# Optimization experiments

Hardware: AMD Instinct MI355X
Metric: run time of the kernel (lower is better)

The kernel has to match this reference:

```python
import jax, jax.numpy as jnp
import numpy as np

B, S, D, H = 4, 4096, 1024, 16
DH = D // H  # 64
EPS = 1e-6


def setup_inputs() -> dict:
    key = jax.random.key(0)
    ks = jax.random.split(key, 6)
    scale = 1.0 / np.sqrt(D).astype(np.float32)
    x = jax.random.normal(ks[0], (B, S, D), jnp.float32)
    # packed cache: rows 0..DH-1 = KV state S0, row DH = normalizer z0 (kept positive)
    state_cache = jax.random.uniform(ks[1], (B, H, DH + 1, DH), jnp.float32)
    Wq = jax.random.normal(ks[2], (D, D), jnp.float32) * scale
    Wk = jax.random.normal(ks[3], (D, D), jnp.float32) * scale
    Wv = jax.random.normal(ks[4], (D, D), jnp.float32) * scale
    Wo = jax.random.normal(ks[5], (D, D), jnp.float32) * scale
    return {"x": x, "state_cache": state_cache, "Wq": Wq, "Wk": Wk, "Wv": Wv, "Wo": Wo}


def reference(x, state_cache, Wq, Wk, Wv, Wo):
    b, s, d = x.shape
    h, dh = H, d // H

    def heads(t):  # [b,s,d] -> [s,b,h,dh] (seq-major for scan)
        return t.reshape(b, s, h, dh).transpose(1, 0, 2, 3)

    phi = lambda t: jax.nn.elu(t) + 1.0  # positive feature map
    q = phi(heads(x @ Wq))
    k = phi(heads(x @ Wk))
    v = heads(x @ Wv)

    S0 = state_cache[:, :, :dh, :]   # [b,h,dh,dh]
    z0 = state_cache[:, :, dh, :]    # [b,h,dh]

    def step(carry, inp):
        Sst, z = carry
        qt, kt, vt = inp  # each [b,h,dh]
        Sst = Sst + jnp.einsum('bhd,bhe->bhde', kt, vt)
        z = z + kt
        num = jnp.einsum('bhd,bhde->bhe', qt, Sst)            # [b,h,dh]
        den = jnp.einsum('bhd,bhd->bh', qt, z)[..., None]     # [b,h,1]
        return (Sst, z), num / (den + EPS)

    _, outs = jax.lax.scan(step, (S0, z0), (q, k, v))  # outs: [s,b,h,dh]
    out = outs.transpose(1, 0, 2, 3).reshape(b, s, d)
    return out @ Wo
```

## Files before the change

kernel.cpp:

```cpp
#include <hip/hip_runtime.h>

#define B_ 4
#define S_ 4096
#define D_ 1024
#define H_ 16
#define DH 64
#define CHUNK 64
#define NC (S_ / CHUNK)
#define BH (B_ * H_)
#define STATE_N 4160
#define EPS 1e-6f

typedef __bf16 bf16;
typedef __bf16 bf16x8 __attribute__((ext_vector_type(8)));
typedef __bf16 bf16x4 __attribute__((ext_vector_type(4)));
typedef float v4f __attribute__((ext_vector_type(4)));

#define MFMA16(a, b, c) __builtin_amdgcn_mfma_f32_16x16x32_bf16(a, b, c, 0, 0, 0)

__device__ __forceinline__ void load_lds16(const bf16* g, bf16* l) {
  __builtin_amdgcn_global_load_lds(
      (const __attribute__((address_space(1))) unsigned int*)g,
      (__attribute__((address_space(3))) unsigned int*)l, 16, 0, 0);
}

__global__ __launch_bounds__(256) void cvt_f32_bf16(const float* __restrict__ in,
                                                    bf16* __restrict__ out) {
  const size_t i = ((size_t)blockIdx.x * 256 + threadIdx.x) * 8;
  float4 a = *(const float4*)(in + i);
  float4 b = *(const float4*)(in + i + 4);
  bf16x8 o;
  o[0] = (bf16)a.x; o[1] = (bf16)a.y; o[2] = (bf16)a.z; o[3] = (bf16)a.w;
  o[4] = (bf16)b.x; o[5] = (bf16)b.y; o[6] = (bf16)b.z; o[7] = (bf16)b.w;
  *(bf16x8*)(out + i) = o;
}

__global__ __launch_bounds__(256) void transpose_w4(
    const float* __restrict__ w0, const float* __restrict__ w1,
    const float* __restrict__ w2, const float* __restrict__ w3,
    bf16* __restrict__ out) {
  __shared__ float tile[32][33];
  const int z = blockIdx.z;
  const float* in = (z == 0) ? w0 : (z == 1) ? w1 : (z == 2) ? w2 : w3;
  bf16* o = out + (size_t)z * D_ * D_;
  const int bx = blockIdx.x * 32, by = blockIdx.y * 32;
  const int tx = threadIdx.x & 31, ty = threadIdx.x >> 5;
#pragma unroll
  for (int i = 0; i < 32; i += 8)
    tile[ty + i][tx] = in[(size_t)(by + ty + i) * D_ + bx + tx];
  __syncthreads();
#pragma unroll
  for (int i = 0; i < 32; i += 8)
    o[(size_t)(bx + ty + i) * D_ + by + tx] = (bf16)tile[tx][ty + i];
}

__global__ __launch_bounds__(256) void gemm_nt(const bf16* __restrict__ A,
                                               const bf16* __restrict__ BT,
                                               bf16* __restrict__ o0,
                                               bf16* __restrict__ o1,
                                               bf16* __restrict__ o2,
                                               float* __restrict__ of) {
  constexpr int TM = 128, BK = 32;
  constexpr int CLD = 132;
  __shared__ __align__(16) char smem[32768];
  float* Cl = (float*)smem;

  const int tid = threadIdx.x;
  const int wave = tid >> 6, lane = tid & 63;
  const int quad = lane >> 4, l16 = lane & 15;
  const int bm = blockIdx.x * TM;
  const int zz = blockIdx.y >> 3;
  const int colg = (blockIdx.y & 7) * 128;
  const int wm = (wave & 1) * 64, wn = (wave >> 1) * 64;
  const int act = (of == nullptr) && (zz < 2);
  bf16* ob = (zz == 0) ? o0 : (zz == 1) ? o1 : o2;

  const int srow = wave * 16 + (lane >> 2);
  const int sgrp = ((lane & 3) - ((lane >> 2) >> 1)) & 3;
  const bf16* gA0 = A + (size_t)(bm + srow) * D_ + sgrp * 8;
  const bf16* gA1 = gA0 + (size_t)64 * D_;
  const bf16* gB0 = BT + ((size_t)blockIdx.y * 128 + srow) * D_ + sgrp * 8;
  const bf16* gB1 = gB0 + (size_t)64 * D_;

  int offA[4], offB[4];
#pragma unroll
  for (int i = 0; i < 4; i++) {
    const int pg = (quad + (l16 >> 1)) & 3;
    offA[i] = (wm + i * 16 + l16) * BK + pg * 8;
    offB[i] = (wn + i * 16 + l16) * BK + pg * 8;
  }

  v4f zero = {0.f, 0.f, 0.f, 0.f};
  v4f acc[4][4];
#pragma unroll
  for (int i = 0; i < 4; i++)
#pragma unroll
    for (int j = 0; j < 4; j++) acc[i][j] = zero;

  auto stage = [&](int ks, int s) {
    bf16* As = (bf16*)(smem + s * 16384);
    bf16* Bs = As + 4096;
    const int ko = ks * BK;
    load_lds16(gA0 + ko, As + wave * 16 * BK);
    load_lds16(gA1 + ko, As + (64 + wave * 16) * BK);
    load_lds16(gB0 + ko, Bs + wave * 16 * BK);
    load_lds16(gB1 + ko, Bs + (64 + wave * 16) * BK);
  };
  auto compute = [&](int s) {
    const bf16* As = (const bf16*)(smem + s * 16384);
    const bf16* Bs = As + 4096;
    bf16x8 af[4], bfr[4];
#pragma unroll
    for (int i = 0; i < 4; i++) af[i] = *(const bf16x8*)&As[offA[i]];
#pragma unroll
    for (int j = 0; j < 4; j++) bfr[j] = *(const bf16x8*)&Bs[offB[j]];
#pragma unroll
    for (int i = 0; i < 4; i++)
#pragma unroll
      for (int j = 0; j < 4; j++) acc[i][j] = MFMA16(af[i], bfr[j], acc[i][j]);
  };

  constexpr int NK = D_ / BK;
  stage(0, 0);
  __syncthreads();
  for (int k = 0; k < NK; k += 2) {
    if (k + 1 < NK) stage(k + 1, 1);
    compute(0);
    __syncthreads();
    if (k + 2 < NK) stage(k + 2, 0);
    compute(1);
    __syncthreads();
  }

  const int lr = (wave & 1) * 16 + quad * 4;
  const int rrow = tid >> 3;
  const int rseg = (tid & 7) * 16;
  const int grow = bm + (rrow >> 4) * 64 + (rrow & 15);
#pragma unroll
  for (int i = 0; i < 4; i++) {
    __syncthreads();
#pragma unroll
    for (int j = 0; j < 4; j++) {
      const int col = wn + j * 16 + l16;
#pragma unroll
      for (int r = 0; r < 4; r++) {
        float x = acc[i][j][r];
        if (act) x = x > 0.f ? x + 1.f : __expf(x);
        Cl[(lr + r) * CLD + col] = x;
      }
    }
    __syncthreads();
    const float* src = &Cl[rrow * CLD + rseg];
    if (of) {
      float* dst = of + (size_t)(grow + i * 16) * D_ + colg + rseg;
#pragma unroll
      for (int u = 0; u < 4; u++)
        *(float4*)(dst + u * 4) = *(const float4*)(src + u * 4);
    } else {
      bf16x8 q0, q1;
#pragma unroll
      for (int u = 0; u < 8; u++) { q0[u] = (bf16)src[u]; q1[u] = (bf16)src[8 + u]; }
      bf16* dst = ob + (size_t)(grow + i * 16) * D_ + colg + rseg;
      *(bf16x8*)dst = q0;
      *(bf16x8*)(dst + 8) = q1;
    }
  }
}

__global__ __launch_bounds__(256) void chunk_kv(const bf16* __restrict__ kb,
                                                const bf16* __restrict__ vb,
                                                float* __restrict__ states) {
  constexpr int LD = 88;
  __shared__ bf16 Kl[CHUNK * LD];
  __shared__ bf16 Vl[CHUNK * LD];
  const int tid = threadIdx.x;
  const int c = blockIdx.x, bh = blockIdx.y;
  const int b = bh >> 4, h = bh & 15;
  const size_t gbase = ((size_t)(b * S_ + c * CHUNK)) * D_ + h * DH;
#pragma unroll
  for (int rep = 0; rep < 2; rep++) {
    int flat = tid + rep * 256;
    int r = flat >> 3, sg = (flat & 7) * 8;
    *(bf16x8*)&Kl[r * LD + sg] = *(const bf16x8*)(kb + gbase + (size_t)r * D_ + sg);
    *(bf16x8*)&Vl[r * LD + sg] = *(const bf16x8*)(vb + gbase + (size_t)r * D_ + sg);
  }
  __syncthreads();
  const int d0 = (tid >> 4) * 4, e0 = (tid & 15) * 4;
  float acc[4][4] = {};
  for (int t = 0; t < CHUNK; t++) {
    bf16x4 k4 = *(const bf16x4*)&Kl[t * LD + d0];
    bf16x4 v4 = *(const bf16x4*)&Vl[t * LD + e0];
    float kf[4], vf[4];
#pragma unroll
    for (int i = 0; i < 4; i++) { kf[i] = (float)k4[i]; vf[i] = (float)v4[i]; }
#pragma unroll
    for (int i = 0; i < 4; i++)
#pragma unroll
      for (int j = 0; j < 4; j++) acc[i][j] += kf[i] * vf[j];
  }
  float* out = states + ((size_t)bh * NC + c) * STATE_N;
#pragma unroll
  for (int i = 0; i < 4; i++)
#pragma unroll
    for (int j = 0; j < 4; j++) out[(d0 + i) * 64 + (e0 + j)] = acc[i][j];
  if (tid < 64) {
    float zs = 0.f;
    for (int t = 0; t < CHUNK; t++) zs += (float)Kl[t * LD + tid];
    out[4096 + tid] = zs;
  }
}

__global__ __launch_bounds__(256) void state_prefix(const float* __restrict__ sc,
                                                    float* __restrict__ states) {
  const int bh = blockIdx.x;
  const int e = blockIdx.y * 256 + threadIdx.x;
  if (e >= STATE_N) return;
  const float* scb = sc + (size_t)bh * (DH + 1) * DH;
  float run = scb[e];
  float* p = states + (size_t)bh * NC * STATE_N + e;
  for (int c = 0; c < NC; c++) {
    float tmp = p[(size_t)c * STATE_N];
    p[(size_t)c * STATE_N] = run;
    run += tmp;
  }
}

__global__ __launch_bounds__(256) void attn_pass2(
    const bf16* __restrict__ qb, const bf16* __restrict__ kb,
    const bf16* __restrict__ vb, const float* __restrict__ states,
    bf16* __restrict__ ao) {
  constexpr int LD = 88;
  __shared__ bf16 Ql[CHUNK * LD];
  __shared__ bf16 Kl[CHUNK * LD];
  __shared__ bf16 VT[DH * LD];
  __shared__ bf16 S0T[DH * LD];
  __shared__ bf16 Pl[CHUNK * LD];
  __shared__ float denl[CHUNK];
  __shared__ float z0l[DH];
  const int tid = threadIdx.x;
  const int wave = tid >> 6, lane = tid & 63;
  const int quad = lane >> 4, l16 = lane & 15;
  const int c = blockIdx.x, bh = blockIdx.y;
  const int b = bh >> 4, h = bh & 15;
  const size_t gbase = ((size_t)(b * S_ + c * CHUNK)) * D_ + h * DH;

#pragma unroll
  for (int rep = 0; rep < 2; rep++) {
    int flat = tid + rep * 256;
    int r = flat >> 3, sg = (flat & 7) * 8;
    *(bf16x8*)&Ql[r * LD + sg] = *(const bf16x8*)(qb + gbase + (size_t)r * D_ + sg);
    *(bf16x8*)&Kl[r * LD + sg] = *(const bf16x8*)(kb + gbase + (size_t)r * D_ + sg);
    bf16x8 vv = *(const bf16x8*)(vb + gbase + (size_t)r * D_ + sg);
#pragma unroll
    for (int u = 0; u < 8; u++) VT[(sg + u) * LD + r] = vv[u];
  }
  const float* st = states + ((size_t)bh * NC + c) * STATE_N;
  for (int f = tid; f < 4096; f += 256) S0T[(f & 63) * LD + (f >> 6)] = (bf16)st[f];
  if (tid < DH) z0l[tid] = st[4096 + tid];
  __syncthreads();

  v4f zero = {0.f, 0.f, 0.f, 0.f};
  v4f pacc[4];
#pragma unroll
  for (int j = 0; j < 4; j++) pacc[j] = zero;
#pragma unroll
  for (int ks = 0; ks < 2; ks++) {
    bf16x8 aq = *(const bf16x8*)&Ql[(wave * 16 + l16) * LD + ks * 32 + quad * 8];
#pragma unroll
    for (int j = 0; j < 4; j++) {
      bf16x8 bk = *(const bf16x8*)&Kl[(j * 16 + l16) * LD + ks * 32 + quad * 8];
      pacc[j] = MFMA16(aq, bk, pacc[j]);
    }
  }
  float rs[4] = {0.f, 0.f, 0.f, 0.f};
#pragma unroll
  for (int j = 0; j < 4; j++) {
#pragma unroll
    for (int r = 0; r < 4; r++) {
      int t = wave * 16 + quad * 4 + r;
      int col = j * 16 + l16;
      float p = (col <= t) ? pacc[j][r] : 0.f;
      Pl[t * LD + col] = (bf16)p;
      rs[r] += p;
    }
  }
#pragma unroll
  for (int m = 1; m < 16; m <<= 1)
#pragma unroll
    for (int r = 0; r < 4; r++) rs[r] += __shfl_xor(rs[r], m, 64);
  if (l16 == 0)
#pragma unroll
    for (int r = 0; r < 4; r++) denl[wave * 16 + quad * 4 + r] = rs[r];
  __syncthreads();
  if (tid < CHUNK) {
    float qz = 0.f;
    for (int d = 0; d < DH; d++) qz += (float)Ql[tid * LD + d] * z0l[d];
    denl[tid] += qz;
  }
  __syncthreads();

  v4f nacc[4];
#pragma unroll
  for (int j = 0; j < 4; j++) nacc[j] = zero;
#pragma unroll
  for (int ks = 0; ks < 2; ks++) {
    bf16x8 ap = *(const bf16x8*)&Pl[(wave * 16 + l16) * LD + ks * 32 + quad * 8];
#pragma unroll
    for (int j = 0; j < 4; j++) {
      bf16x8 bv = *(const bf16x8*)&VT[(j * 16 + l16) * LD + ks * 32 + quad * 8];
      nacc[j] = MFMA16(ap, bv, nacc[j]);
    }
  }
#pragma unroll
  for (int ks = 0; ks < 2; ks++) {
    bf16x8 aq = *(const bf16x8*)&Ql[(wave * 16 + l16) * LD + ks * 32 + quad * 8];
#pragma unroll
    for (int j = 0; j < 4; j++) {
      bf16x8 bs = *(const bf16x8*)&S0T[(j * 16 + l16) * LD + ks * 32 + quad * 8];
      nacc[j] = MFMA16(aq, bs, nacc[j]);
    }
  }
#pragma unroll
  for (int j = 0; j < 4; j++) {
#pragma unroll
    for (int r = 0; r < 4; r++) {
      int t = wave * 16 + quad * 4 + r;
      int e = j * 16 + l16;
      float o = nacc[j][r] / (denl[t] + EPS);
      ao[gbase + (size_t)t * D_ + e] = (bf16)o;
    }
  }
}

extern "C" void kernel_launch(void* const* d_in, const int* in_sizes, int n_in,
                              void* d_out, int out_size, void* d_ws, size_t ws_size,
                              hipStream_t stream) {
  const float* x  = (const float*)d_in[0];
  const float* sc = (const float*)d_in[1];
  const float* Wq = (const float*)d_in[2];
  const float* Wk = (const float*)d_in[3];
  const float* Wv = (const float*)d_in[4];
  const float* Wo = (const float*)d_in[5];
  float* out = (float*)d_out;

  const size_t MSZ = (size_t)B_ * S_ * D_;
  const size_t WSZ = (size_t)D_ * D_;
  bf16* xb = (bf16*)d_ws;
  bf16* qb = xb + MSZ;
  bf16* kb = qb + MSZ;
  bf16* vb = kb + MSZ;
  bf16* ao = vb + MSZ;
  bf16* wt = ao + MSZ;
  float* states = (float*)(wt + 4 * WSZ);

  cvt_f32_bf16<<<MSZ / (256 * 8), 256, 0, stream>>>(x, xb);
  transpose_w4<<<dim3(32, 32, 4), 256, 0, stream>>>(Wq, Wk, Wv, Wo, wt);

  gemm_nt<<<dim3(128, 24), 256, 0, stream>>>(xb, wt, qb, kb, vb, nullptr);

  chunk_kv<<<dim3(NC, BH), 256, 0, stream>>>(kb, vb, states);
  state_prefix<<<dim3(BH, 17), 256, 0, stream>>>(sc, states);
  attn_pass2<<<dim3(NC, BH), 256, 0, stream>>>(qb, kb, vb, states, ao);

  gemm_nt<<<dim3(128, 8), 256, 0, stream>>>(ao, wt + 3 * WSZ, nullptr, nullptr,
                                            nullptr, out);
}
```

Baseline: 428.0 us.

## Replace GEMM with 256x256-tile 8-wave kernel with phased LDS pipeline

Replaces the 128x128-tile, 4-wave GEMM with a 256x256-tile, 512-thread kernel that uses BK=64 and XOR-swizzled LDS layouts. Each k-step is split into four phases that interleave async global-to-LDS loads with MFMA blocks, using explicit vmcnt waits, barriers and setprio. The larger tile is meant to raise arithmetic intensity and keep the matrix cores busy while loads are in flight. In exchange it uses 128KB of LDS and more registers per block, and the launch grids shrink to 768 and 256 blocks, which can leave CUs underused.

Result: slower. 1.018 ms (+137.9%).

```diff
diff --git a/kernel.cpp b/kernel.cpp
--- a/kernel.cpp
+++ b/kernel.cpp
@@ -54,116 +54,154 @@
     o[(size_t)(bx + ty + i) * D_ + by + tx] = (bf16)tile[tx][ty + i];
 }
 
-__global__ __launch_bounds__(256) void gemm_nt(const bf16* __restrict__ A,
-                                               const bf16* __restrict__ BT,
-                                               bf16* __restrict__ o0,
-                                               bf16* __restrict__ o1,
-                                               bf16* __restrict__ o2,
-                                               float* __restrict__ of) {
-  constexpr int TM = 128, BK = 32;
-  constexpr int CLD = 132;
-  __shared__ __align__(16) char smem[32768];
-  float* Cl = (float*)smem;
-
+#define PHASE(S, MH, NH, LA, LB, STMT, WN)                                     \
+  do {                                                                         \
+    if (LA) {                                                                  \
+      _Pragma("unroll") for (int m = 0; m < 4; m++) {                          \
+        aR[m][0] = *(const bf16x8*)&lds[(S)*16384 + (MH)*8192 + m*512 + aoff]; \
+        aR[m][1] = *(const bf16x8*)&lds[(S)*16384 + (MH)*8192 + 4096 + m*512 + aoff]; \
+      }                                                                        \
+    }                                                                          \
+    if (LB) {                                                                  \
+      _Pragma("unroll") for (int n = 0; n < 2; n++) {                          \
+        bR[NH][n][0] = *(const bf16x8*)&lds[(S)*16384 + (NH)*8192 + n*512 + boff]; \
+        bR[NH][n][1] = *(const bf16x8*)&lds[(S)*16384 + (NH)*8192 + 4096 + n*512 + boff]; \
+      }                                                                        \
+    }                                                                          \
+    STMT;                                                                      \
+    if ((WN) == 4) asm volatile("s_waitcnt vmcnt(4)" ::: "memory");            \
+    else if ((WN) == 2) asm volatile("s_waitcnt vmcnt(2)" ::: "memory");       \
+    else if ((WN) == 0) asm volatile("s_waitcnt vmcnt(0)" ::: "memory");       \
+    __builtin_amdgcn_s_barrier();                                              \
+    __builtin_amdgcn_s_setprio(1);                                             \
+    _Pragma("unroll") for (int ks = 0; ks < 2; ks++)                           \
+      _Pragma("unroll") for (int m = 0; m < 4; m++)                            \
+        _Pragma("unroll") for (int n = 0; n < 2; n++)                          \
+          acc[MH][m][NH][n] = MFMA16(aR[m][ks], bR[NH][n][ks], acc[MH][m][NH][n]); \
+    __builtin_amdgcn_s_setprio(0);                                             \
+    __builtin_amdgcn_s_barrier();                                              \
+  } while (0)
+
+__global__ __launch_bounds__(512, 2) void gemm256(const bf16* __restrict__ A,
+                                                  const bf16* __restrict__ BT,
+                                                  bf16* __restrict__ o0,
+                                                  bf16* __restrict__ o1,
+                                                  bf16* __restrict__ o2,
+                                                  float* __restrict__ of) {
+  __shared__ __align__(16) bf16 lds[65536];
   const int tid = threadIdx.x;
-  const int wave = tid >> 6, lane = tid & 63;
+  const int wv = tid >> 6, lane = tid & 63;
   const int quad = lane >> 4, l16 = lane & 15;
-  const int bm = blockIdx.x * TM;
-  const int zz = blockIdx.y >> 3;
-  const int colg = (blockIdx.y & 7) * 128;
-  const int wm = (wave & 1) * 64, wn = (wave >> 1) * 64;
+  const int wr = wv >> 2, wc = wv & 3;
+  const int bm = blockIdx.x * 256;
+  const int by = blockIdx.y;
+  const int zz = of ? 0 : (by >> 2);
+  const int colg = of ? by * 256 : (by & 3) * 256;
   const int act = (of == nullptr) && (zz < 2);
   bf16* ob = (zz == 0) ? o0 : (zz == 1) ? o1 : o2;
 
-  const int srow = wave * 16 + (lane >> 2);
-  const int sgrp = ((lane & 3) - ((lane >> 2) >> 1)) & 3;
-  const bf16* gA0 = A + (size_t)(bm + srow) * D_ + sgrp * 8;
-  const bf16* gA1 = gA0 + (size_t)64 * D_;
-  const bf16* gB0 = BT + ((size_t)blockIdx.y * 128 + srow) * D_ + sgrp * 8;
-  const bf16* gB1 = gB0 + (size_t)64 * D_;
-
-  int offA[4], offB[4];
+  const int r = tid >> 2;
+  const int gsw = (tid & 3) ^ ((r >> 2) & 3);
+  const bf16* sA0 = A + (size_t)(bm + r) * D_ + gsw * 8;
+  const bf16* sA1 = A + (size_t)(bm + 128 + r) * D_ + gsw * 8;
+  const bf16* sB0 = BT + ((size_t)by * 256 + r) * D_ + gsw * 8;
+  const bf16* sB1 = BT + ((size_t)by * 256 + 128 + r) * D_ + gsw * 8;
+
+  auto stageA = [&](int h, int kt, int s) {
+    const bf16* src = (h ? sA1 : sA0) + kt * 64;
+    bf16* d = &lds[s * 16384 + h * 8192 + wv * 512];
+    load_lds16(src, d);
+    load_lds16(src + 32, d + 4096);
+  };
+  auto stageB = [&](int h, int kt, int s) {
+    const bf16* src = (h ? sB1 : sB0) + kt * 64;
+    bf16* d = &lds[32768 + s * 16384 + h * 8192 + wv * 512];
+    load_lds16(src, d);
+    load_lds16(src + 32, d + 4096);
+  };
+
+  const int qsw = quad ^ ((l16 >> 2) & 3);
+  const int aoff = (wr * 64 + l16) * 32 + qsw * 8;
+  const int boff = 32768 + (wc * 32 + l16) * 32 + qsw * 8;
+
+  v4f acc[2][4][2][2];
+#pragma unroll
+  for (int a0 = 0; a0 < 2; a0++)
+#pragma unroll
+    for (int a1 = 0; a1 < 4; a1++)
+#pragma unroll
+      for (int a2 = 0; a2 < 2; a2++)
+#pragma unroll
+        for (int a3 = 0; a3 < 2; a3++) acc[a0][a1][a2][a3] = (v4f){0.f, 0.f, 0.f, 0.f};
+  bf16x8 aR[4][2];
+  bf16x8 bR[2][2][2];
+
+  stageA(0, 0, 0); stageB(0, 0, 0); stageB(1, 0, 0); stageA(1, 0, 0);
+  asm volatile("s_waitcnt vmcnt(4)" ::: "memory");
+  __builtin_amdgcn_s_barrier();
+
+  constexpr int NK = D_ / 64;
+#pragma unroll 1
+  for (int t = 0; t < NK; t += 2) {
+    PHASE(0, 0, 0, 1, 1, stageA(0, t + 1, 1), 4);
+    PHASE(0, 0, 1, 0, 1, stageB(0, t + 1, 1), 4);
+    PHASE(0, 1, 1, 1, 0, stageB(1, t + 1, 1), -1);
+    PHASE(0, 1, 0, 0, 0, stageA(1, t + 1, 1), 4);
+    if (t + 2 < NK) {
+      PHASE(1, 0, 0, 1, 1, stageA(0, t + 2, 0), 4);
+      PHASE(1, 0, 1, 0, 1, stageB(0, t + 2, 0), 4);
+      PHASE(1, 1, 1, 1, 0, stageB(1, t + 2, 0), -1);
+      PHASE(1, 1, 0, 0, 0, stageA(1, t + 2, 0), 4);
+    } else {
+      PHASE(1, 0, 0, 1, 1, (void)0, 2);
+      PHASE(1, 0, 1, 0, 1, (void)0, 0);
+      PHASE(1, 1, 1, 1, 0, (void)0, -1);
+      PHASE(1, 1, 0, 0, 0, (void)0, -1);
+    }
+  }
+
+  __syncthreads();
+  float* Cl = (float*)lds;
+  const int erow = tid >> 3;
+  const int wrr = erow >> 5, mrow = erow & 31;
+  const int seg = (tid & 7) * 32;
 #pragma unroll
   for (int i = 0; i < 4; i++) {
-    const int pg = (quad + (l16 >> 1)) & 3;
-    offA[i] = (wm + i * 16 + l16) * BK + pg * 8;
-    offB[i] = (wn + i * 16 + l16) * BK + pg * 8;
-  }
-
-  v4f zero = {0.f, 0.f, 0.f, 0.f};
-  v4f acc[4][4];
-#pragma unroll
-  for (int i = 0; i < 4; i++)
-#pragma unroll
-    for (int j = 0; j < 4; j++) acc[i][j] = zero;
-
-  auto stage = [&](int ks, int s) {
-    bf16* As = (bf16*)(smem + s * 16384);
-    bf16* Bs = As + 4096;
-    const int ko = ks * BK;
-    load_lds16(gA0 + ko, As + wave * 16 * BK);
-    load_lds16(gA1 + ko, As + (64 + wave * 16) * BK);
-    load_lds16(gB0 + ko, Bs + wave * 16 * BK);
-    load_lds16(gB1 + ko, Bs + (64 + wave * 16) * BK);
-  };
-  auto compute = [&](int s) {
-    const bf16* As = (const bf16*)(smem + s * 16384);
-    const bf16* Bs = As + 4096;
-    bf16x8 af[4], bfr[4];
-#pragma unroll
-    for (int i = 0; i < 4; i++) af[i] = *(const bf16x8*)&As[offA[i]];
-#pragma unroll
-    for (int j = 0; j < 4; j++) bfr[j] = *(const bf16x8*)&Bs[offB[j]];
-#pragma unroll
-    for (int i = 0; i < 4; i++)
-#pragma unroll
-      for (int j = 0; j < 4; j++) acc[i][j] = MFMA16(af[i], bfr[j], acc[i][j]);
-  };
-
-  constexpr int NK = D_ / BK;
-  stage(0, 0);
-  __syncthreads();
-  for (int k = 0; k < NK; k += 2) {
-    if (k + 1 < NK) stage(k + 1, 1);
-    compute(0);
+    const int mh = i >> 1, mp = i & 1;
+#pragma unroll
+    for (int mm = 0; mm < 2; mm++) {
+      const int m = mp * 2 + mm;
+#pragma unroll
+      for (int nh = 0; nh < 2; nh++)
+#pragma unroll
+        for (int n = 0; n < 2; n++)
+#pragma unroll
+          for (int rr = 0; rr < 4; rr++) {
+            float x = acc[mh][m][nh][n][rr];
+            if (act) x = x > 0.f ? x + 1.f : __expf(x);
+            Cl[(wr * 32 + mm * 16 + quad * 4 + rr) * 260 +
+               nh * 128 + wc * 32 + n * 16 + l16] = x;
+          }
+    }
     __syncthreads();
-    if (k + 2 < NK) stage(k + 2, 0);
-    compute(1);
+    const float* srcp = &Cl[(wrr * 32 + mrow) * 260 + seg];
+    const size_t grow = (size_t)(bm + mh * 128 + wrr * 64 + mp * 32 + mrow);
+    if (of) {
+      float* dst = of + grow * D_ + colg + seg;
+#pragma unroll
+      for (int u = 0; u < 8; u++)
+        *(float4*)(dst + u * 4) = *(const float4*)(srcp + u * 4);
+    } else {
+      bf16* dst = ob + grow * D_ + colg + seg;
+#pragma unroll
+      for (int u = 0; u < 4; u++) {
+        bf16x8 q;
+#pragma unroll
+        for (int e = 0; e < 8; e++) q[e] = (bf16)srcp[u * 8 + e];
+        *(bf16x8*)(dst + u * 8) = q;
+      }
+    }
     __syncthreads();
-  }
-
-  const int lr = (wave & 1) * 16 + quad * 4;
-  const int rrow = tid >> 3;
-  const int rseg = (tid & 7) * 16;
-  const int grow = bm + (rrow >> 4) * 64 + (rrow & 15);
-#pragma unroll
-  for (int i = 0; i < 4; i++) {
-    __syncthreads();
-#pragma unroll
-    for (int j = 0; j < 4; j++) {
-      const int col = wn + j * 16 + l16;
-#pragma unroll
-      for (int r = 0; r < 4; r++) {
-        float x = acc[i][j][r];
-        if (act) x = x > 0.f ? x + 1.f : __expf(x);
-        Cl[(lr + r) * CLD + col] = x;
-      }
-    }
-    __syncthreads();
-    const float* src = &Cl[rrow * CLD + rseg];
-    if (of) {
-      float* dst = of + (size_t)(grow + i * 16) * D_ + colg + rseg;
-#pragma unroll
-      for (int u = 0; u < 4; u++)
-        *(float4*)(dst + u * 4) = *(const float4*)(src + u * 4);
-    } else {
-      bf16x8 q0, q1;
-#pragma unroll
-      for (int u = 0; u < 8; u++) { q0[u] = (bf16)src[u]; q1[u] = (bf16)src[8 + u]; }
-      bf16* dst = ob + (size_t)(grow + i * 16) * D_ + colg + rseg;
-      *(bf16x8*)dst = q0;
-      *(bf16x8*)(dst + 8) = q1;
-    }
   }
 }
 
@@ -180,9 +218,9 @@
 #pragma unroll
   for (int rep = 0; rep < 2; rep++) {
     int flat = tid + rep * 256;
-    int r = flat >> 3, sg = (flat & 7) * 8;
-    *(bf16x8*)&Kl[r * LD + sg] = *(const bf16x8*)(kb + gbase + (size_t)r * D_ + sg);
-    *(bf16x8*)&Vl[r * LD + sg] = *(const bf16x8*)(vb + gbase + (size_t)r * D_ + sg);
+    int rr = flat >> 3, sg = (flat & 7) * 8;
+    *(bf16x8*)&Kl[rr * LD + sg] = *(const bf16x8*)(kb + gbase + (size_t)rr * D_ + sg);
+    *(bf16x8*)&Vl[rr * LD + sg] = *(const bf16x8*)(vb + gbase + (size_t)rr * D_ + sg);
   }
   __syncthreads();
   const int d0 = (tid >> 4) * 4, e0 = (tid & 15) * 4;
@@ -247,12 +285,12 @@
 #pragma unroll
   for (int rep = 0; rep < 2; rep++) {
     int flat = tid + rep * 256;
-    int r = flat >> 3, sg = (flat & 7) * 8;
-    *(bf16x8*)&Ql[r * LD + sg] = *(const bf16x8*)(qb + gbase + (size_t)r * D_ + sg);
-    *(bf16x8*)&Kl[r * LD + sg] = *(const bf16x8*)(kb + gbase + (size_t)r * D_ + sg);
-    bf16x8 vv = *(const bf16x8*)(vb + gbase + (size_t)r * D_ + sg);
-#pragma unroll
-    for (int u = 0; u < 8; u++) VT[(sg + u) * LD + r] = vv[u];
+    int rr = flat >> 3, sg = (flat & 7) * 8;
+    *(bf16x8*)&Ql[rr * LD + sg] = *(const bf16x8*)(qb + gbase + (size_t)rr * D_ + sg);
+    *(bf16x8*)&Kl[rr * LD + sg] = *(const bf16x8*)(kb + gbase + (size_t)rr * D_ + sg);
+    bf16x8 vv = *(const bf16x8*)(vb + gbase + (size_t)rr * D_ + sg);
+#pragma unroll
+    for (int u = 0; u < 8; u++) VT[(sg + u) * LD + rr] = vv[u];
   }
   const float* st = states + ((size_t)bh * NC + c) * STATE_N;
   for (int f = tid; f < 4096; f += 256) S0T[(f & 63) * LD + (f >> 6)] = (bf16)st[f];
@@ -276,21 +314,21 @@
 #pragma unroll
   for (int j = 0; j < 4; j++) {
 #pragma unroll
-    for (int r = 0; r < 4; r++) {
-      int t = wave * 16 + quad * 4 + r;
+    for (int rr = 0; rr < 4; rr++) {
+      int t = wave * 16 + quad * 4 + rr;
       int col = j * 16 + l16;
-      float p = (col <= t) ? pacc[j][r] : 0.f;
+      float p = (col <= t) ? pacc[j][rr] : 0.f;
       Pl[t * LD + col] = (bf16)p;
-      rs[r] += p;
+      rs[rr] += p;
     }
   }
 #pragma unroll
   for (int m = 1; m < 16; m <<= 1)
 #pragma unroll
-    for (int r = 0; r < 4; r++) rs[r] += __shfl_xor(rs[r], m, 64);
+    for (int rr = 0; rr < 4; rr++) rs[rr] += __shfl_xor(rs[rr], m, 64);
   if (l16 == 0)
 #pragma unroll
-    for (int r = 0; r < 4; r++) denl[wave * 16 + quad * 4 + r] = rs[r];
+    for (int rr = 0; rr < 4; rr++) denl[wave * 16 + quad * 4 + rr] = rs[rr];
   __syncthreads();
   if (tid < CHUNK) {
     float qz = 0.f;
@@ -323,10 +361,10 @@
 #pragma unroll
   for (int j = 0; j < 4; j++) {
 #pragma unroll
-    for (int r = 0; r < 4; r++) {
-      int t = wave * 16 + quad * 4 + r;
+    for (int rr = 0; rr < 4; rr++) {
+      int t = wave * 16 + quad * 4 + rr;
       int e = j * 16 + l16;
-      float o = nacc[j][r] / (denl[t] + EPS);
+      float o = nacc[j][rr] / (denl[t] + EPS);
       ao[gbase + (size_t)t * D_ + e] = (bf16)o;
     }
   }
@@ -356,12 +394,12 @@
   cvt_f32_bf16<<<MSZ / (256 * 8), 256, 0, stream>>>(x, xb);
   transpose_w4<<<dim3(32, 32, 4), 256, 0, stream>>>(Wq, Wk, Wv, Wo, wt);
 
-  gemm_nt<<<dim3(128, 24), 256, 0, stream>>>(xb, wt, qb, kb, vb, nullptr);
+  gemm256<<<dim3(64, 12), 512, 0, stream>>>(xb, wt, qb, kb, vb, nullptr);
 
   chunk_kv<<<dim3(NC, BH), 256, 0, stream>>>(kb, vb, states);
   state_prefix<<<dim3(BH, 17), 256, 0, stream>>>(sc, states);
   attn_pass2<<<dim3(NC, BH), 256, 0, stream>>>(qb, kb, vb, states, ao);
 
-  gemm_nt<<<dim3(128, 8), 256, 0, stream>>>(ao, wt + 3 * WSZ, nullptr, nullptr,
-                                            nullptr, out);
-}
+  gemm256<<<dim3(64, 4), 512, 0, stream>>>(ao, wt + 3 * WSZ, nullptr, nullptr,
+                                           nullptr, out);
+}
```

## Fuse chunk state, prefix scan and attention into one sequential-chunk kernel

Applied to the files above, without the earlier changes.

Replaces three kernels (per-chunk KV outer products, global prefix over chunk states, per-chunk attention) with one kernel. Each block walks all 64 chunks of one (batch, head, 16-column slice) in order, keeping the running state in MFMA accumulator registers and double-buffering the next chunk's Q/K/V loads. LDS uses XOR-swizzled layouts. This removes the float state buffer round-trips through global memory and two launches. In exchange it uses only 256 blocks with a long serial chain per block, and recomputes QK^T four times per chunk because the head is split across four blocks by output slice.

New measurement: 442.9 us. 3.5% more time.

```diff
diff --git a/kernel.cpp b/kernel.cpp
--- a/kernel.cpp
+++ b/kernel.cpp
@@ -8,12 +8,10 @@
 #define CHUNK 64
 #define NC (S_ / CHUNK)
 #define BH (B_ * H_)
-#define STATE_N 4160
 #define EPS 1e-6f
 
 typedef __bf16 bf16;
 typedef __bf16 bf16x8 __attribute__((ext_vector_type(8)));
-typedef __bf16 bf16x4 __attribute__((ext_vector_type(4)));
 typedef float v4f __attribute__((ext_vector_type(4)));
 
 #define MFMA16(a, b, c) __builtin_amdgcn_mfma_f32_16x16x32_bf16(a, b, c, 0, 0, 0)
@@ -22,6 +20,10 @@
   __builtin_amdgcn_global_load_lds(
       (const __attribute__((address_space(1))) unsigned int*)g,
       (__attribute__((address_space(3))) unsigned int*)l, 16, 0, 0);
+}
+
+__device__ __forceinline__ int swz72(int row, int col) {
+  return row * 72 + ((((col >> 3) ^ (row >> 3)) & 7) << 3) + (col & 7);
 }
 
 __global__ __launch_bounds__(256) void cvt_f32_bf16(const float* __restrict__ in,
@@ -167,168 +169,185 @@
   }
 }
 
-__global__ __launch_bounds__(256) void chunk_kv(const bf16* __restrict__ kb,
-                                                const bf16* __restrict__ vb,
-                                                float* __restrict__ states) {
-  constexpr int LD = 88;
-  __shared__ bf16 Kl[CHUNK * LD];
-  __shared__ bf16 Vl[CHUNK * LD];
-  const int tid = threadIdx.x;
-  const int c = blockIdx.x, bh = blockIdx.y;
-  const int b = bh >> 4, h = bh & 15;
-  const size_t gbase = ((size_t)(b * S_ + c * CHUNK)) * D_ + h * DH;
-#pragma unroll
-  for (int rep = 0; rep < 2; rep++) {
-    int flat = tid + rep * 256;
-    int r = flat >> 3, sg = (flat & 7) * 8;
-    *(bf16x8*)&Kl[r * LD + sg] = *(const bf16x8*)(kb + gbase + (size_t)r * D_ + sg);
-    *(bf16x8*)&Vl[r * LD + sg] = *(const bf16x8*)(vb + gbase + (size_t)r * D_ + sg);
-  }
-  __syncthreads();
-  const int d0 = (tid >> 4) * 4, e0 = (tid & 15) * 4;
-  float acc[4][4] = {};
-  for (int t = 0; t < CHUNK; t++) {
-    bf16x4 k4 = *(const bf16x4*)&Kl[t * LD + d0];
-    bf16x4 v4 = *(const bf16x4*)&Vl[t * LD + e0];
-    float kf[4], vf[4];
-#pragma unroll
-    for (int i = 0; i < 4; i++) { kf[i] = (float)k4[i]; vf[i] = (float)v4[i]; }
-#pragma unroll
-    for (int i = 0; i < 4; i++)
-#pragma unroll
-      for (int j = 0; j < 4; j++) acc[i][j] += kf[i] * vf[j];
-  }
-  float* out = states + ((size_t)bh * NC + c) * STATE_N;
-#pragma unroll
-  for (int i = 0; i < 4; i++)
-#pragma unroll
-    for (int j = 0; j < 4; j++) out[(d0 + i) * 64 + (e0 + j)] = acc[i][j];
-  if (tid < 64) {
-    float zs = 0.f;
-    for (int t = 0; t < CHUNK; t++) zs += (float)Kl[t * LD + tid];
-    out[4096 + tid] = zs;
-  }
-}
-
-__global__ __launch_bounds__(256) void state_prefix(const float* __restrict__ sc,
-                                                    float* __restrict__ states) {
-  const int bh = blockIdx.x;
-  const int e = blockIdx.y * 256 + threadIdx.x;
-  if (e >= STATE_N) return;
-  const float* scb = sc + (size_t)bh * (DH + 1) * DH;
-  float run = scb[e];
-  float* p = states + (size_t)bh * NC * STATE_N + e;
-  for (int c = 0; c < NC; c++) {
-    float tmp = p[(size_t)c * STATE_N];
-    p[(size_t)c * STATE_N] = run;
-    run += tmp;
-  }
-}
-
-__global__ __launch_bounds__(256) void attn_pass2(
+__global__ __launch_bounds__(256) void fused_scan(
     const bf16* __restrict__ qb, const bf16* __restrict__ kb,
-    const bf16* __restrict__ vb, const float* __restrict__ states,
+    const bf16* __restrict__ vb, const float* __restrict__ sc,
     bf16* __restrict__ ao) {
-  constexpr int LD = 88;
-  __shared__ bf16 Ql[CHUNK * LD];
-  __shared__ bf16 Kl[CHUNK * LD];
-  __shared__ bf16 VT[DH * LD];
-  __shared__ bf16 S0T[DH * LD];
-  __shared__ bf16 Pl[CHUNK * LD];
+  __shared__ __align__(16) bf16 Ql[2][CHUNK * 72];
+  __shared__ __align__(16) bf16 Kl[2][CHUNK * 72];
+  __shared__ __align__(16) bf16 KT[2][CHUNK * 72];
+  __shared__ __align__(16) bf16 VT[2][16 * 72];
+  __shared__ __align__(16) bf16 S0T[16 * 72];
+  __shared__ __align__(16) bf16 Pl[CHUNK * 72];
+  __shared__ __align__(16) bf16 Ol[CHUNK * 72];
+  __shared__ float zl[DH];
   __shared__ float denl[CHUNK];
-  __shared__ float z0l[DH];
+
   const int tid = threadIdx.x;
   const int wave = tid >> 6, lane = tid & 63;
   const int quad = lane >> 4, l16 = lane & 15;
-  const int c = blockIdx.x, bh = blockIdx.y;
+  const int r8 = blockIdx.x & 7, q8 = blockIdx.x >> 3;
+  const int bh = r8 * 8 + (q8 >> 2), es = q8 & 3;
   const int b = bh >> 4, h = bh & 15;
-  const size_t gbase = ((size_t)(b * S_ + c * CHUNK)) * D_ + h * DH;
-
-#pragma unroll
-  for (int rep = 0; rep < 2; rep++) {
-    int flat = tid + rep * 256;
-    int r = flat >> 3, sg = (flat & 7) * 8;
-    *(bf16x8*)&Ql[r * LD + sg] = *(const bf16x8*)(qb + gbase + (size_t)r * D_ + sg);
-    *(bf16x8*)&Kl[r * LD + sg] = *(const bf16x8*)(kb + gbase + (size_t)r * D_ + sg);
-    bf16x8 vv = *(const bf16x8*)(vb + gbase + (size_t)r * D_ + sg);
-#pragma unroll
-    for (int u = 0; u < 8; u++) VT[(sg + u) * LD + r] = vv[u];
-  }
-  const float* st = states + ((size_t)bh * NC + c) * STATE_N;
-  for (int f = tid; f < 4096; f += 256) S0T[(f & 63) * LD + (f >> 6)] = (bf16)st[f];
-  if (tid < DH) z0l[tid] = st[4096 + tid];
+
+  const float* scb = sc + (size_t)bh * (DH + 1) * DH;
+  v4f S_frag;
+#pragma unroll
+  for (int r = 0; r < 4; r++)
+    S_frag[r] = scb[(wave * 16 + quad * 4 + r) * 64 + es * 16 + l16];
+  if (tid < DH) zl[tid] = scb[4096 + tid];
+
+  const int sr = tid >> 3, sg = (tid & 7) * 8;
+  const int vrow = tid >> 1, ve8 = (tid & 1) * 8;
+  const size_t seqbase = ((size_t)(b * S_)) * D_ + h * DH;
+
+  {
+    bf16x8 rq0 = *(const bf16x8*)(qb + seqbase + (size_t)sr * D_ + sg);
+    bf16x8 rq1 = *(const bf16x8*)(qb + seqbase + (size_t)(sr + 32) * D_ + sg);
+    bf16x8 rk0 = *(const bf16x8*)(kb + seqbase + (size_t)sr * D_ + sg);
+    bf16x8 rk1 = *(const bf16x8*)(kb + seqbase + (size_t)(sr + 32) * D_ + sg);
+    *(bf16x8*)&Ql[0][sr * 72 + sg] = rq0;
+    *(bf16x8*)&Ql[0][(sr + 32) * 72 + sg] = rq1;
+    *(bf16x8*)&Kl[0][sr * 72 + sg] = rk0;
+    *(bf16x8*)&Kl[0][(sr + 32) * 72 + sg] = rk1;
+#pragma unroll
+    for (int u = 0; u < 8; u++) {
+      KT[0][swz72(sg + u, sr)] = rk0[u];
+      KT[0][swz72(sg + u, sr + 32)] = rk1[u];
+    }
+    if (tid < 128) {
+      bf16x8 rv = *(const bf16x8*)(vb + seqbase + (size_t)vrow * D_ + es * 16 + ve8);
+#pragma unroll
+      for (int u = 0; u < 8; u++) VT[0][swz72(ve8 + u, vrow)] = rv[u];
+    }
+  }
   __syncthreads();
 
-  v4f zero = {0.f, 0.f, 0.f, 0.f};
-  v4f pacc[4];
-#pragma unroll
-  for (int j = 0; j < 4; j++) pacc[j] = zero;
-#pragma unroll
-  for (int ks = 0; ks < 2; ks++) {
-    bf16x8 aq = *(const bf16x8*)&Ql[(wave * 16 + l16) * LD + ks * 32 + quad * 8];
-#pragma unroll
-    for (int j = 0; j < 4; j++) {
-      bf16x8 bk = *(const bf16x8*)&Kl[(j * 16 + l16) * LD + ks * 32 + quad * 8];
-      pacc[j] = MFMA16(aq, bk, pacc[j]);
-    }
-  }
-  float rs[4] = {0.f, 0.f, 0.f, 0.f};
-#pragma unroll
-  for (int j = 0; j < 4; j++) {
+  const v4f zero = {0.f, 0.f, 0.f, 0.f};
+#pragma unroll 2
+  for (int c = 0; c < NC; c++) {
+    const int cur = c & 1, nxt = cur ^ 1;
+    const size_t cb = seqbase + (size_t)(c * 64) * D_;
+    const bool more = (c + 1 < NC);
+
+    bf16x8 rq0 = {}, rq1 = {}, rk0 = {}, rk1 = {}, rv = {};
+    if (more) {
+      const size_t nb = cb + (size_t)64 * D_;
+      rq0 = *(const bf16x8*)(qb + nb + (size_t)sr * D_ + sg);
+      rq1 = *(const bf16x8*)(qb + nb + (size_t)(sr + 32) * D_ + sg);
+      rk0 = *(const bf16x8*)(kb + nb + (size_t)sr * D_ + sg);
+      rk1 = *(const bf16x8*)(kb + nb + (size_t)(sr + 32) * D_ + sg);
+      if (tid < 128)
+        rv = *(const bf16x8*)(vb + nb + (size_t)vrow * D_ + es * 16 + ve8);
+    }
+    if (c > 0 && tid < 128) {
+      bf16x8 o8 = *(const bf16x8*)&Ol[swz72(vrow, ve8)];
+      *(bf16x8*)(ao + cb - (size_t)64 * D_ + (size_t)vrow * D_ + es * 16 + ve8) = o8;
+    }
+#pragma unroll
+    for (int r = 0; r < 4; r++)
+      S0T[swz72(l16, wave * 16 + quad * 4 + r)] = (bf16)S_frag[r];
+    bf16x8 aq[2];
+    v4f pacc[4];
+#pragma unroll
+    for (int j = 0; j < 4; j++) pacc[j] = zero;
+#pragma unroll
+    for (int ks = 0; ks < 2; ks++) {
+      aq[ks] = *(const bf16x8*)&Ql[cur][(wave * 16 + l16) * 72 + ks * 32 + quad * 8];
+#pragma unroll
+      for (int j = 0; j < 4; j++) {
+        bf16x8 bk = *(const bf16x8*)&Kl[cur][(j * 16 + l16) * 72 + ks * 32 + quad * 8];
+        pacc[j] = MFMA16(aq[ks], bk, pacc[j]);
+      }
+    }
+    float rs[4] = {0.f, 0.f, 0.f, 0.f};
+#pragma unroll
+    for (int j = 0; j < 4; j++)
+#pragma unroll
+      for (int r = 0; r < 4; r++) {
+        int t = wave * 16 + quad * 4 + r;
+        int col = j * 16 + l16;
+        float p = (col <= t) ? pacc[j][r] : 0.f;
+        Pl[swz72(t, col)] = (bf16)p;
+        rs[r] += p;
+      }
+#pragma unroll
+    for (int m = 1; m < 16; m <<= 1)
+#pragma unroll
+      for (int r = 0; r < 4; r++) rs[r] += __shfl_xor(rs[r], m, 64);
+    if (l16 == 0)
+#pragma unroll
+      for (int r = 0; r < 4; r++) denl[wave * 16 + quad * 4 + r] = rs[r];
+    __syncthreads();
+
+    {
+      const int t = tid >> 2, p = tid & 3;
+      bf16x8 qa = *(const bf16x8*)&Ql[cur][t * 72 + p * 16];
+      bf16x8 qb2 = *(const bf16x8*)&Ql[cur][t * 72 + p * 16 + 8];
+      float qz = 0.f;
+#pragma unroll
+      for (int u = 0; u < 8; u++)
+        qz += (float)qa[u] * zl[p * 16 + u] + (float)qb2[u] * zl[p * 16 + 8 + u];
+      qz += __shfl_xor(qz, 1, 64);
+      qz += __shfl_xor(qz, 2, 64);
+      if (p == 0) denl[t] += qz;
+    }
+    v4f nacc = zero;
+    bf16x8 bvv[2];
+#pragma unroll
+    for (int ks = 0; ks < 2; ks++) {
+      bvv[ks] = *(const bf16x8*)&VT[cur][swz72(l16, ks * 32 + quad * 8)];
+      bf16x8 ap = *(const bf16x8*)&Pl[swz72(wave * 16 + l16, ks * 32 + quad * 8)];
+      nacc = MFMA16(ap, bvv[ks], nacc);
+    }
+#pragma unroll
+    for (int ks = 0; ks < 2; ks++) {
+      bf16x8 bs = *(const bf16x8*)&S0T[swz72(l16, ks * 32 + quad * 8)];
+      nacc = MFMA16(aq[ks], bs, nacc);
+    }
+    __syncthreads();
+
+#pragma unroll
+    for (int ks = 0; ks < 2; ks++) {
+      bf16x8 ak = *(const bf16x8*)&KT[cur][swz72(wave * 16 + l16, ks * 32 + quad * 8)];
+      S_frag = MFMA16(ak, bvv[ks], S_frag);
+    }
+    {
+      const int d = tid >> 2, p = tid & 3;
+      bf16x8 a0 = *(const bf16x8*)&KT[cur][swz72(d, p * 16)];
+      bf16x8 a1 = *(const bf16x8*)&KT[cur][swz72(d, p * 16 + 8)];
+      float zp = 0.f;
+#pragma unroll
+      for (int u = 0; u < 8; u++) zp += (float)a0[u] + (float)a1[u];
+      zp += __shfl_xor(zp, 1, 64);
+      zp += __shfl_xor(zp, 2, 64);
+      if (p == 0) zl[d] += zp;
+    }
 #pragma unroll
     for (int r = 0; r < 4; r++) {
       int t = wave * 16 + quad * 4 + r;
-      int col = j * 16 + l16;
-      float p = (col <= t) ? pacc[j][r] : 0.f;
-      Pl[t * LD + col] = (bf16)p;
-      rs[r] += p;
-    }
-  }
-#pragma unroll
-  for (int m = 1; m < 16; m <<= 1)
-#pragma unroll
-    for (int r = 0; r < 4; r++) rs[r] += __shfl_xor(rs[r], m, 64);
-  if (l16 == 0)
-#pragma unroll
-    for (int r = 0; r < 4; r++) denl[wave * 16 + quad * 4 + r] = rs[r];
-  __syncthreads();
-  if (tid < CHUNK) {
-    float qz = 0.f;
-    for (int d = 0; d < DH; d++) qz += (float)Ql[tid * LD + d] * z0l[d];
-    denl[tid] += qz;
-  }
-  __syncthreads();
-
-  v4f nacc[4];
-#pragma unroll
-  for (int j = 0; j < 4; j++) nacc[j] = zero;
-#pragma unroll
-  for (int ks = 0; ks < 2; ks++) {
-    bf16x8 ap = *(const bf16x8*)&Pl[(wave * 16 + l16) * LD + ks * 32 + quad * 8];
-#pragma unroll
-    for (int j = 0; j < 4; j++) {
-      bf16x8 bv = *(const bf16x8*)&VT[(j * 16 + l16) * LD + ks * 32 + quad * 8];
-      nacc[j] = MFMA16(ap, bv, nacc[j]);
-    }
-  }
-#pragma unroll
-  for (int ks = 0; ks < 2; ks++) {
-    bf16x8 aq = *(const bf16x8*)&Ql[(wave * 16 + l16) * LD + ks * 32 + quad * 8];
-#pragma unroll
-    for (int j = 0; j < 4; j++) {
-      bf16x8 bs = *(const bf16x8*)&S0T[(j * 16 + l16) * LD + ks * 32 + quad * 8];
-      nacc[j] = MFMA16(aq, bs, nacc[j]);
-    }
-  }
-#pragma unroll
-  for (int j = 0; j < 4; j++) {
-#pragma unroll
-    for (int r = 0; r < 4; r++) {
-      int t = wave * 16 + quad * 4 + r;
-      int e = j * 16 + l16;
-      float o = nacc[j][r] / (denl[t] + EPS);
-      ao[gbase + (size_t)t * D_ + e] = (bf16)o;
-    }
+      Ol[swz72(t, l16)] = (bf16)(nacc[r] / (denl[t] + EPS));
+    }
+    if (more) {
+      *(bf16x8*)&Ql[nxt][sr * 72 + sg] = rq0;
+      *(bf16x8*)&Ql[nxt][(sr + 32) * 72 + sg] = rq1;
+      *(bf16x8*)&Kl[nxt][sr * 72 + sg] = rk0;
+      *(bf16x8*)&Kl[nxt][(sr + 32) * 72 + sg] = rk1;
+#pragma unroll
+      for (int u = 0; u < 8; u++) {
+        KT[nxt][swz72(sg + u, sr)] = rk0[u];
+        KT[nxt][swz72(sg + u, sr + 32)] = rk1[u];
+      }
+      if (tid < 128)
+#pragma unroll
+        for (int u = 0; u < 8; u++) VT[nxt][swz72(ve8 + u, vrow)] = rv[u];
+    }
+    __syncthreads();
+  }
+  if (tid < 128) {
+    const size_t cb = seqbase + (size_t)((NC - 1) * 64) * D_;
+    bf16x8 o8 = *(const bf16x8*)&Ol[swz72(vrow, ve8)];
+    *(bf16x8*)(ao + cb + (size_t)vrow * D_ + es * 16 + ve8) = o8;
   }
 }
 
@@ -351,16 +370,13 @@
   bf16* vb = kb + MSZ;
   bf16* ao = vb + MSZ;
   bf16* wt = ao + MSZ;
-  float* states = (float*)(wt + 4 * WSZ);
 
   cvt_f32_bf16<<<MSZ / (256 * 8), 256, 0, stream>>>(x, xb);
   transpose_w4<<<dim3(32, 32, 4), 256, 0, stream>>>(Wq, Wk, Wv, Wo, wt);
 
   gemm_nt<<<dim3(128, 24), 256, 0, stream>>>(xb, wt, qb, kb, vb, nullptr);
 
-  chunk_kv<<<dim3(NC, BH), 256, 0, stream>>>(kb, vb, states);
-  state_prefix<<<dim3(BH, 17), 256, 0, stream>>>(sc, states);
-  attn_pass2<<<dim3(NC, BH), 256, 0, stream>>>(qb, kb, vb, states, ao);
+  fused_scan<<<256, 256, 0, stream>>>(qb, kb, vb, sc, ao);
 
   gemm_nt<<<dim3(128, 8), 256, 0, stream>>>(ao, wt + 3 * WSZ, nullptr, nullptr,
                                             nullptr, out);
```
